# Optimization experiments

Measured on AMD Instinct MI355X. Metric: run time of the kernel, lower is better.

The kernel has to match this reference:

```python
import jax, jax.numpy as jnp
import numpy as np

B, U, C, M = 4096, 1024, 5000, 20

def setup_inputs() -> dict:
    key = jax.random.key(0)
    ks = jax.random.split(key, 9)
    inputs = jax.random.randint(ks[0], (B, 1), 0, C).astype(jnp.int32)
    states = 0.1 * jax.random.normal(ks[1], (B, U + 2), dtype=jnp.float32)
    bias_z = jnp.zeros((U,), jnp.float32)
    recurrent_kernel = 0.02 * jax.random.normal(ks[2], (U, 4 * U), dtype=jnp.float32)
    kernel_c = 0.02 * jax.random.normal(ks[3], (C, 4 * U), dtype=jnp.float32)
    bias = jnp.zeros((3 * U,), jnp.float32)
    kernel_d = 0.1 * jax.random.normal(ks[4], (2, 4 * U), dtype=jnp.float32)
    Wgmm_part1 = 0.05 * jax.random.normal(ks[5], (U, 3 * M), dtype=jnp.float32)
    bgmm_part1 = jnp.zeros((3 * M,), jnp.float32)
    return {"inputs": inputs, "states": states, "bias_z": bias_z,
            "recurrent_kernel": recurrent_kernel, "kernel_c": kernel_c,
            "bias": bias, "kernel_d": kernel_d,
            "Wgmm_part1": Wgmm_part1, "bgmm_part1": bgmm_part1}

def exp_safe(x):
    return jnp.clip(jnp.exp(x), 1e-10, 1e10)

def reference(inputs, states, bias_z, recurrent_kernel, kernel_c, bias,
              kernel_d, Wgmm_part1, bgmm_part1):
    u = bias_z.shape[0]
    h_tm1 = states[:, :-2]          # [B, U]
    _d = states[:, -2:]             # [B, 2]
    ch = inputs[:, 0].astype(jnp.int32)
    # one_hot(ch) @ kernel_c is just a row gather
    pre = kernel_c[ch] + _d @ kernel_d              # [B, 4U]
    # z and r gates share the left operand -> fuse into one matmul
    zr = (h_tm1 @ recurrent_kernel[:, :2 * u] + pre[:, :2 * u]
          + jnp.concatenate([bias_z, bias[:u]]))
    z = jax.nn.sigmoid(zr[:, :u])
    r = jax.nn.sigmoid(zr[:, u:])
    hh = jnp.tanh((r * h_tm1) @ recurrent_kernel[:, 2 * u:3 * u]
                  + pre[:, 2 * u:3 * u] + bias[u:2 * u])
    h = z * h_tm1 + (1.0 - z) * hh
    o = jnp.tanh(h @ recurrent_kernel[:, 3 * u:]
                 + pre[:, 3 * u:] + bias[2 * u:])
    gmm = o @ Wgmm_part1 + bgmm_part1               # [B, 3M]
    _pi, mux, muy = jnp.split(gmm, 3, axis=-1)
    e = exp_safe(_pi)
    pi = e / jnp.sum(e, axis=-1, keepdims=True)
    x_pred = jnp.sum(pi * mux, axis=-1, keepdims=True)
    y_pred = jnp.sum(pi * muy, axis=-1, keepdims=True)
    out = jnp.concatenate([o, pi, mux, muy, x_pred, y_pred], axis=-1)
    new_state = jnp.concatenate([h, x_pred, y_pred], axis=-1)
    return out, new_state
```

## Files before the change

kernel.cpp:

```cpp
#include <hip/hip_runtime.h>

typedef __attribute__((ext_vector_type(8))) short     bf16x8;
typedef __attribute__((ext_vector_type(4))) float     f32x4;
typedef __attribute__((ext_vector_type(2))) float     f32x2;
typedef __attribute__((ext_vector_type(4))) unsigned short u16x4;

#define OUT_STRIDE 1086
#define NS_STRIDE 1026
#define NS_BASE (4096*1086)

__device__ __forceinline__ unsigned short f2bf(float x) {
  unsigned int u = __float_as_uint(x);
  unsigned int r = (u + 0x7FFFu + ((u >> 16) & 1u)) >> 16;
  return (unsigned short)r;
}
__device__ __forceinline__ float bf2f(unsigned short u) {
  union { unsigned int i; float f; } v; v.i = ((unsigned int)u) << 16; return v.f;
}
__device__ __forceinline__ float sigmoidf(float x) { return 1.f / (1.f + expf(-x)); }

__device__ __forceinline__ void gld_lds16(const void* g, void* l) {
  __builtin_amdgcn_global_load_lds((const __attribute__((address_space(1))) void*)g,
                                   (__attribute__((address_space(3))) void*)l, 16, 0, 0);
}

__device__ __forceinline__ void decode_block(int bid, int& m0, int& n0) {
  const int swz = (bid & 7) * 64 + (bid >> 3);
  const int chunk = swz >> 6, l = swz & 63;
  m0 = ((chunk & 3) * 8 + (l >> 3)) * 128;
  n0 = ((chunk >> 2) * 8 + (l & 7)) * 64;
}

__global__ __launch_bounds__(256)
void transposeR(const float* __restrict__ R, unsigned short* __restrict__ Bt) {
  __shared__ float t[64][65];
  const int tx = threadIdx.x & 63, ty = threadIdx.x >> 6;
  const int j0 = blockIdx.x * 64, k0 = blockIdx.y * 64;
#pragma unroll
  for (int i = 0; i < 64; i += 4)
    t[ty + i][tx] = R[(size_t)(k0 + ty + i) * 4096 + j0 + tx];
  __syncthreads();
#pragma unroll
  for (int i = 0; i < 64; i += 4) {
    const int j = ty + i;
    Bt[(size_t)(j0 + j) * 1024 + k0 + tx] = f2bf(t[tx][j]);
  }
}

__global__ __launch_bounds__(256)
void convertH(const float* __restrict__ states, unsigned short* __restrict__ hb) {
  const int idx = blockIdx.x * 256 + threadIdx.x;
  const int b = idx >> 8, u = (idx & 255) * 4;
  const float* sp = states + (size_t)b * 1026 + u;
  f32x2 v0 = *(const f32x2*)sp, v1 = *(const f32x2*)(sp + 2);
  u16x4 w;
  w[0] = f2bf(v0[0]); w[1] = f2bf(v0[1]); w[2] = f2bf(v1[0]); w[3] = f2bf(v1[1]);
  *(u16x4*)&hb[(size_t)b * 1024 + u] = w;
}

__global__ __launch_bounds__(256)
void gemm_zr(const unsigned short* __restrict__ A,
             const unsigned short* __restrict__ Bt,
             const int* __restrict__ chv,
             const float* __restrict__ states,
             const float* __restrict__ kc,
             const float* __restrict__ kd,
             const float* __restrict__ bias_z,
             const float* __restrict__ bias,
             float* __restrict__ zbuf,
             unsigned short* __restrict__ rh) {
  __shared__ unsigned short Al[4][128 * 32];
  __shared__ unsigned short Bzl[4][64 * 32];
  __shared__ unsigned short Brl[4][64 * 32];
  __shared__ int   chs[128];
  __shared__ float d0s[128], d1s[128];

  const int tid = threadIdx.x, lane = tid & 63, wave = tid >> 6;
  int m0, n0;
  decode_block(blockIdx.x, m0, n0);

  if (tid < 128) {
    const int r = m0 + tid;
    chs[tid] = chv[r];
    d0s[tid] = states[(size_t)r * 1026 + 1024];
    d1s[tid] = states[(size_t)r * 1026 + 1025];
  }

  const unsigned short* Ag  = A  + (size_t)m0 * 1024;
  const unsigned short* Bzg = Bt + (size_t)n0 * 1024;
  const unsigned short* Brg = Bt + (size_t)(1024 + n0) * 1024;

  const int c1 = tid + 256;
  const int ar0 = tid >> 2, ak0 = (tid & 3) * 8;
  const int ar1 = c1 >> 2,  ak1 = (c1 & 3) * 8;

  f32x4 accz[2][4] = {}, accr[2][4] = {};
  const int arow = lane & 15, kg = (lane >> 4) * 8;

#define STAGE_ZR(b, kk)                                                        \
  gld_lds16(Ag  + (size_t)ar0 * 1024 + (kk) + ak0, &Al[b][tid * 8]);           \
  gld_lds16(Ag  + (size_t)ar1 * 1024 + (kk) + ak1, &Al[b][c1 * 8]);            \
  gld_lds16(Bzg + (size_t)ar0 * 1024 + (kk) + ak0, &Bzl[b][tid * 8]);          \
  gld_lds16(Brg + (size_t)ar0 * 1024 + (kk) + ak0, &Brl[b][tid * 8]);

  auto compute = [&](int cb) {
    bf16x8 af[2], bzf[4], brf[4];
#pragma unroll
    for (int mi = 0; mi < 2; ++mi)
      af[mi] = *(const bf16x8*)&Al[cb][(wave * 32 + mi * 16 + arow) * 32 + kg];
#pragma unroll
    for (int ni = 0; ni < 4; ++ni) {
      bzf[ni] = *(const bf16x8*)&Bzl[cb][(ni * 16 + arow) * 32 + kg];
      brf[ni] = *(const bf16x8*)&Brl[cb][(ni * 16 + arow) * 32 + kg];
    }
    __builtin_amdgcn_s_setprio(1);
#pragma unroll
    for (int mi = 0; mi < 2; ++mi)
#pragma unroll
      for (int ni = 0; ni < 4; ++ni) {
        accz[mi][ni] = __builtin_amdgcn_mfma_f32_16x16x32_bf16(af[mi], bzf[ni], accz[mi][ni], 0, 0, 0);
        accr[mi][ni] = __builtin_amdgcn_mfma_f32_16x16x32_bf16(af[mi], brf[ni], accr[mi][ni], 0, 0, 0);
      }
    __builtin_amdgcn_s_setprio(0);
  };

  STAGE_ZR(0, 0);
  STAGE_ZR(1, 32);
  for (int t = 0; t < 30; ++t) {
    const int nx = (t + 2) & 3;
    STAGE_ZR(nx, (t + 2) * 32);
    asm volatile("s_waitcnt vmcnt(8)" ::: "memory");
    __builtin_amdgcn_s_barrier();
    asm volatile("" ::: "memory");
    compute(t & 3);
  }
  asm volatile("s_waitcnt vmcnt(4)" ::: "memory");
  __builtin_amdgcn_s_barrier();
  asm volatile("" ::: "memory");
  compute(2);
  asm volatile("s_waitcnt vmcnt(0)" ::: "memory");
  __builtin_amdgcn_s_barrier();
  asm volatile("" ::: "memory");
  compute(3);
#undef STAGE_ZR

#pragma unroll
  for (int mi = 0; mi < 2; ++mi) {
#pragma unroll
    for (int r = 0; r < 4; ++r) {
      const int lrow = wave * 32 + mi * 16 + (lane >> 4) * 4 + r;
      const int grow = m0 + lrow;
      const int ch = chs[lrow];
      const float d0 = d0s[lrow], d1 = d1s[lrow];
      const float* kcrow = kc + (size_t)ch * 4096;
#pragma unroll
      for (int ni = 0; ni < 4; ++ni) {
        const int jc = n0 + ni * 16 + (lane & 15);
        const float vz = accz[mi][ni][r] + kcrow[jc]
                       + d0 * kd[jc] + d1 * kd[4096 + jc] + bias_z[jc];
        const float vr = accr[mi][ni][r] + kcrow[1024 + jc]
                       + d0 * kd[1024 + jc] + d1 * kd[4096 + 1024 + jc] + bias[jc];
        const float z = sigmoidf(vz);
        const float rr = sigmoidf(vr);
        zbuf[(size_t)grow * 1024 + jc] = z;
        rh[(size_t)grow * 1024 + jc] = f2bf(rr * bf2f(A[(size_t)grow * 1024 + jc]));
      }
    }
  }
}

template<int EPI>
__global__ __launch_bounds__(256)
void gemm_k(const unsigned short* __restrict__ A,
            const unsigned short* __restrict__ Bt,
            const int* __restrict__ chv,
            const float* __restrict__ states,
            const float* __restrict__ kc, int colbase,
            const float* __restrict__ kd,
            const float* __restrict__ bias, int biasoff,
            const float* __restrict__ zbuf,
            float* __restrict__ out2,
            unsigned short* __restrict__ hb2) {
  __shared__ unsigned short Al[4][128 * 32];
  __shared__ unsigned short Bl[4][64 * 32];
  __shared__ int   chs[128];
  __shared__ float d0s[128], d1s[128];

  const int tid = threadIdx.x, lane = tid & 63, wave = tid >> 6;
  int m0, n0;
  decode_block(blockIdx.x, m0, n0);

  if (tid < 128) {
    const int r = m0 + tid;
    chs[tid] = chv[r];
    d0s[tid] = states[(size_t)r * 1026 + 1024];
    d1s[tid] = states[(size_t)r * 1026 + 1025];
  }

  const unsigned short* Ag = A  + (size_t)m0 * 1024;
  const unsigned short* Bg = Bt + (size_t)n0 * 1024;

  const int c1 = tid + 256;
  const int ar0 = tid >> 2, ak0 = (tid & 3) * 8;
  const int ar1 = c1 >> 2,  ak1 = (c1 & 3) * 8;

  f32x4 acc[2][4] = {};
  const int arow = lane & 15, kg = (lane >> 4) * 8;

#define STAGE_K(b, kk)                                                         \
  gld_lds16(Ag + (size_t)ar0 * 1024 + (kk) + ak0, &Al[b][tid * 8]);            \
  gld_lds16(Ag + (size_t)ar1 * 1024 + (kk) + ak1, &Al[b][c1 * 8]);             \
  gld_lds16(Bg + (size_t)ar0 * 1024 + (kk) + ak0, &Bl[b][tid * 8]);

  auto compute = [&](int cb) {
    bf16x8 af[2], bfr[4];
#pragma unroll
    for (int mi = 0; mi < 2; ++mi)
      af[mi] = *(const bf16x8*)&Al[cb][(wave * 32 + mi * 16 + arow) * 32 + kg];
#pragma unroll
    for (int ni = 0; ni < 4; ++ni)
      bfr[ni] = *(const bf16x8*)&Bl[cb][(ni * 16 + arow) * 32 + kg];
    __builtin_amdgcn_s_setprio(1);
#pragma unroll
    for (int mi = 0; mi < 2; ++mi)
#pragma unroll
      for (int ni = 0; ni < 4; ++ni)
        acc[mi][ni] = __builtin_amdgcn_mfma_f32_16x16x32_bf16(af[mi], bfr[ni], acc[mi][ni], 0, 0, 0);
    __builtin_amdgcn_s_setprio(0);
  };

  STAGE_K(0, 0);
  STAGE_K(1, 32);
  for (int t = 0; t < 30; ++t) {
    const int nx = (t + 2) & 3;
    STAGE_K(nx, (t + 2) * 32);
    asm volatile("s_waitcnt vmcnt(6)" ::: "memory");
    __builtin_amdgcn_s_barrier();
    asm volatile("" ::: "memory");
    compute(t & 3);
  }
  asm volatile("s_waitcnt vmcnt(3)" ::: "memory");
  __builtin_amdgcn_s_barrier();
  asm volatile("" ::: "memory");
  compute(2);
  asm volatile("s_waitcnt vmcnt(0)" ::: "memory");
  __builtin_amdgcn_s_barrier();
  asm volatile("" ::: "memory");
  compute(3);
#undef STAGE_K

#pragma unroll
  for (int mi = 0; mi < 2; ++mi) {
#pragma unroll
    for (int r = 0; r < 4; ++r) {
      const int lrow = wave * 32 + mi * 16 + (lane >> 4) * 4 + r;
      const int grow = m0 + lrow;
      const int ch = chs[lrow];
      const float d0 = d0s[lrow], d1 = d1s[lrow];
      const float* kcrow = kc + (size_t)ch * 4096 + colbase;
#pragma unroll
      for (int ni = 0; ni < 4; ++ni) {
        const int gcol = n0 + ni * 16 + (lane & 15);
        float v = acc[mi][ni][r] + kcrow[gcol]
                + d0 * kd[colbase + gcol] + d1 * kd[4096 + colbase + gcol]
                + bias[biasoff + gcol];
        if (EPI == 2) {
          const float hh = tanhf(v);
          const float z = zbuf[(size_t)grow * 1024 + gcol];
          const float htm = states[(size_t)grow * 1026 + gcol];
          const float h = z * htm + (1.f - z) * hh;
          out2[(size_t)grow * NS_STRIDE + gcol] = h;
          hb2[(size_t)grow * 1024 + gcol] = f2bf(h);
        } else {
          out2[(size_t)grow * OUT_STRIDE + gcol] = tanhf(v);
        }
      }
    }
  }
}

__global__ __launch_bounds__(512)
void gmm_kernel(const float* __restrict__ obuf,
                const float* __restrict__ Wg,
                const float* __restrict__ bg,
                float* __restrict__ outp,
                float* __restrict__ ns) {
  __shared__ float Wl[128 * 60 + 16];
  __shared__ float ol[8 * 1024];
  const int tid = threadIdx.x;
  const int lane = tid & 63;
  const int wave = tid >> 6;
  const int row0 = blockIdx.x * 8;

  for (int i = tid; i < 4096; i += 512) {
    const int rr = i >> 9, c2 = (i & 511) * 2;
    *(f32x2*)&ol[rr * 1024 + c2] = *(const f32x2*)&obuf[(size_t)(row0 + rr) * OUT_STRIDE + c2];
  }

  float g = 0.f;
  for (int kc0 = 0; kc0 < 1024; kc0 += 128) {
    __syncthreads();
    for (int i = tid; i < 1920; i += 512)
      *(f32x4*)&Wl[i * 4] = *(const f32x4*)&Wg[kc0 * 60 + i * 4];
    __syncthreads();
    const float* orow = &ol[wave * 1024 + kc0];
#pragma unroll 8
    for (int k = 0; k < 128; ++k)
      g = fmaf(orow[k], Wl[k * 60 + lane], g);
  }
  if (lane < 60) g += bg[lane];

  float e = 0.f;
  if (lane < 20) e = fminf(fmaxf(expf(g), 1e-10f), 1e10f);
  float s = e;
#pragma unroll
  for (int m = 1; m < 32; m <<= 1) s += __shfl_xor(s, m, 64);
  const float pi = (lane < 20) ? e / s : 0.f;
  const int src1 = (lane < 20) ? lane + 20 : lane;
  const int src2 = (lane < 20) ? lane + 40 : lane;
  const float mux = __shfl(g, src1, 64);
  const float muy = __shfl(g, src2, 64);
  float px = pi * mux, py = pi * muy;
#pragma unroll
  for (int m = 1; m < 32; m <<= 1) { px += __shfl_xor(px, m, 64); py += __shfl_xor(py, m, 64); }

  const int row = row0 + wave;
  float* orow = outp + (size_t)row * OUT_STRIDE;
  if (lane < 20) orow[1024 + lane] = pi;
  else if (lane < 60) orow[1024 + lane] = g;
  if (lane == 0) {
    orow[1084] = px;
    orow[1085] = py;
    ns[(size_t)row * NS_STRIDE + 1024] = px;
    ns[(size_t)row * NS_STRIDE + 1025] = py;
  }
}

extern "C" void kernel_launch(void* const* d_in, const int* in_sizes, int n_in,
                              void* d_out, int out_size, void* d_ws, size_t ws_size,
                              hipStream_t stream) {
  const int*   chv    = (const int*)d_in[0];
  const float* states = (const float*)d_in[1];
  const float* bias_z = (const float*)d_in[2];
  const float* R      = (const float*)d_in[3];
  const float* kc     = (const float*)d_in[4];
  const float* bias   = (const float*)d_in[5];
  const float* kd     = (const float*)d_in[6];
  const float* Wg     = (const float*)d_in[7];
  const float* bg     = (const float*)d_in[8];
  float* out = (float*)d_out;

  char* ws = (char*)d_ws;
  unsigned short* RbT  = (unsigned short*)ws;
  unsigned short* hb   = (unsigned short*)(ws + 8388608);
  unsigned short* rh   = (unsigned short*)(ws + 16777216);
  unsigned short* hb2  = (unsigned short*)(ws + 25165824);
  float*          zbuf = (float*)(ws + 33554432);

  transposeR<<<dim3(64, 16), 256, 0, stream>>>(R, RbT);
  convertH<<<4096, 256, 0, stream>>>(states, hb);

  gemm_zr<<<512, 256, 0, stream>>>(hb, RbT, chv, states, kc, kd, bias_z, bias, zbuf, rh);

  gemm_k<2><<<512, 256, 0, stream>>>(rh, RbT + (size_t)2048 * 1024,
      chv, states, kc, 2048, kd, bias, 1024, zbuf, out + NS_BASE, hb2);

  gemm_k<3><<<512, 256, 0, stream>>>(hb2, RbT + (size_t)3072 * 1024,
      chv, states, kc, 3072, kd, bias, 2048, nullptr, out, nullptr);

  gmm_kernel<<<512, 512, 0, stream>>>(out, Wg, bg, out, out + NS_BASE);
}
```

Baseline: 328.7 us.

## Compute GMM head with bf16 MFMA using bf16 copy of o and transposed weights

The output-gate GEMM epilogue now also writes a bf16 copy of o into the reused hb buffer. A new prep kernel transposes and pads Wgmm to 64 columns in bf16. The fp32 LDS-based GMM kernel is replaced by an MFMA 16x16x32 kernel that splits K across four waves, reduces the partials through shared memory, and runs the softmax and mixture sums on the MFMA output layout. This targets the scalar FMA cost of the small head GEMM, at the price of bf16 rounding on o and Wgmm and one extra kernel launch.

```diff
diff --git a/kernel.cpp b/kernel.cpp
--- a/kernel.cpp
+++ b/kernel.cpp
@@ -56,6 +56,17 @@
   u16x4 w;
   w[0] = f2bf(v0[0]); w[1] = f2bf(v0[1]); w[2] = f2bf(v1[0]); w[3] = f2bf(v1[1]);
   *(u16x4*)&hb[(size_t)b * 1024 + u] = w;
+}
+
+__global__ __launch_bounds__(256)
+void prep_wgt(const float* __restrict__ Wg, unsigned short* __restrict__ WgT) {
+  const int idx = blockIdx.x * 256 + threadIdx.x;
+  const int c = idx & 63, kq = idx >> 6;
+#pragma unroll
+  for (int j = 0; j < 4; ++j) {
+    const int k = kq * 4 + j;
+    WgT[(size_t)c * 1024 + k] = (c < 60) ? f2bf(Wg[(size_t)k * 60 + c]) : (unsigned short)0;
+  }
 }
 
 __global__ __launch_bounds__(256)
@@ -272,67 +283,104 @@
           out2[(size_t)grow * NS_STRIDE + gcol] = h;
           hb2[(size_t)grow * 1024 + gcol] = f2bf(h);
         } else {
-          out2[(size_t)grow * OUT_STRIDE + gcol] = tanhf(v);
+          const float o = tanhf(v);
+          out2[(size_t)grow * OUT_STRIDE + gcol] = o;
+          hb2[(size_t)grow * 1024 + gcol] = f2bf(o);
         }
       }
     }
   }
 }
 
-__global__ __launch_bounds__(512)
-void gmm_kernel(const float* __restrict__ obuf,
-                const float* __restrict__ Wg,
-                const float* __restrict__ bg,
-                float* __restrict__ outp,
-                float* __restrict__ ns) {
-  __shared__ float Wl[128 * 60 + 16];
-  __shared__ float ol[8 * 1024];
-  const int tid = threadIdx.x;
-  const int lane = tid & 63;
-  const int wave = tid >> 6;
-  const int row0 = blockIdx.x * 8;
-
-  for (int i = tid; i < 4096; i += 512) {
-    const int rr = i >> 9, c2 = (i & 511) * 2;
-    *(f32x2*)&ol[rr * 1024 + c2] = *(const f32x2*)&obuf[(size_t)(row0 + rr) * OUT_STRIDE + c2];
-  }
-
-  float g = 0.f;
-  for (int kc0 = 0; kc0 < 1024; kc0 += 128) {
-    __syncthreads();
-    for (int i = tid; i < 1920; i += 512)
-      *(f32x4*)&Wl[i * 4] = *(const f32x4*)&Wg[kc0 * 60 + i * 4];
-    __syncthreads();
-    const float* orow = &ol[wave * 1024 + kc0];
-#pragma unroll 8
-    for (int k = 0; k < 128; ++k)
-      g = fmaf(orow[k], Wl[k * 60 + lane], g);
-  }
-  if (lane < 60) g += bg[lane];
-
-  float e = 0.f;
-  if (lane < 20) e = fminf(fmaxf(expf(g), 1e-10f), 1e10f);
-  float s = e;
-#pragma unroll
-  for (int m = 1; m < 32; m <<= 1) s += __shfl_xor(s, m, 64);
-  const float pi = (lane < 20) ? e / s : 0.f;
-  const int src1 = (lane < 20) ? lane + 20 : lane;
-  const int src2 = (lane < 20) ? lane + 40 : lane;
-  const float mux = __shfl(g, src1, 64);
-  const float muy = __shfl(g, src2, 64);
-  float px = pi * mux, py = pi * muy;
-#pragma unroll
-  for (int m = 1; m < 32; m <<= 1) { px += __shfl_xor(px, m, 64); py += __shfl_xor(py, m, 64); }
-
-  const int row = row0 + wave;
-  float* orow = outp + (size_t)row * OUT_STRIDE;
-  if (lane < 20) orow[1024 + lane] = pi;
-  else if (lane < 60) orow[1024 + lane] = g;
-  if (lane == 0) {
-    orow[1084] = px;
-    orow[1085] = py;
-    ns[(size_t)row * NS_STRIDE + 1024] = px;
-    ns[(size_t)row * NS_STRIDE + 1025] = py;
+__global__ __launch_bounds__(256)
+void gmm2(const unsigned short* __restrict__ ob,
+          const unsigned short* __restrict__ WgT,
+          const float* __restrict__ bg,
+          float* __restrict__ outp,
+          float* __restrict__ ns) {
+  __shared__ float red[3 * 16 * 64];
+  const int tid = threadIdx.x, lane = tid & 63, wave = tid >> 6;
+  const int arow = lane & 15, q = lane >> 4;
+  const int r0 = blockIdx.x * 16;
+
+  const unsigned short* Al = ob  + (size_t)(r0 + arow) * 1024 + q * 8 + wave * 256;
+  const unsigned short* Bl = WgT + (size_t)arow * 1024 + q * 8 + wave * 256;
+
+  f32x4 acc[4] = {};
+#pragma unroll
+  for (int t = 0; t < 8; ++t) {
+    const bf16x8 af = *(const bf16x8*)(Al + t * 32);
+#pragma unroll
+    for (int ni = 0; ni < 4; ++ni) {
+      const bf16x8 bf_ = *(const bf16x8*)(Bl + (size_t)ni * 16 * 1024 + t * 32);
+      acc[ni] = __builtin_amdgcn_mfma_f32_16x16x32_bf16(af, bf_, acc[ni], 0, 0, 0);
+    }
+  }
+
+  if (wave) {
+#pragma unroll
+    for (int ni = 0; ni < 4; ++ni)
+#pragma unroll
+      for (int i = 0; i < 4; ++i)
+        red[(wave - 1) * 1024 + (ni * 4 + i) * 64 + lane] = acc[ni][i];
+  }
+  __syncthreads();
+  if (wave == 0) {
+#pragma unroll
+    for (int w = 0; w < 3; ++w)
+#pragma unroll
+      for (int ni = 0; ni < 4; ++ni)
+#pragma unroll
+        for (int i = 0; i < 4; ++i)
+          acc[ni][i] += red[w * 1024 + (ni * 4 + i) * 64 + lane];
+
+    const int gb = lane & 48;
+#pragma unroll
+    for (int i = 0; i < 4; ++i) {
+      float g0 = acc[0][i] + bg[arow];
+      float g1 = acc[1][i] + ((16 + arow < 60) ? bg[16 + arow] : 0.f);
+      float g2 = acc[2][i] + ((32 + arow < 60) ? bg[32 + arow] : 0.f);
+      float g3 = acc[3][i] + ((48 + arow < 60) ? bg[48 + arow] : 0.f);
+
+      const float e0 = fminf(fmaxf(expf(g0), 1e-10f), 1e10f);
+      const float e1 = (arow < 4) ? fminf(fmaxf(expf(g1), 1e-10f), 1e10f) : 0.f;
+      float s = e0 + e1;
+#pragma unroll
+      for (int m = 1; m < 16; m <<= 1) s += __shfl_xor(s, m, 64);
+      const float pi0 = e0 / s;
+      const float pi1 = e1 / s;
+
+      const float t1 = __shfl(g1, gb | ((arow + 4) & 15), 64);
+      const float t2 = __shfl(g2, gb | ((arow + 4) & 15), 64);
+      const float muxA = (arow < 12) ? t1 : t2;
+      const float muxB = t2;
+      const float u1 = __shfl(g2, gb | ((arow + 8) & 15), 64);
+      const float u2 = __shfl(g3, gb | ((arow + 8) & 15), 64);
+      const float muyA = (arow < 8) ? u1 : u2;
+      const float muyB = u2;
+
+      float px = pi0 * muxA + ((arow < 4) ? pi1 * muxB : 0.f);
+      float py = pi0 * muyA + ((arow < 4) ? pi1 * muyB : 0.f);
+#pragma unroll
+      for (int m = 1; m < 16; m <<= 1) {
+        px += __shfl_xor(px, m, 64);
+        py += __shfl_xor(py, m, 64);
+      }
+
+      const int row = r0 + q * 4 + i;
+      float* orow = outp + (size_t)row * OUT_STRIDE;
+      orow[1024 + arow] = pi0;
+      if (arow < 4)  orow[1040 + arow] = pi1;
+      if (arow >= 4) orow[1040 + arow] = g1;
+      orow[1056 + arow] = g2;
+      if (arow < 12) orow[1072 + arow] = g3;
+      if (arow == 0) {
+        orow[1084] = px;
+        orow[1085] = py;
+        ns[(size_t)row * NS_STRIDE + 1024] = px;
+        ns[(size_t)row * NS_STRIDE + 1025] = py;
+      }
+    }
   }
 }
 
@@ -356,9 +404,11 @@
   unsigned short* rh   = (unsigned short*)(ws + 16777216);
   unsigned short* hb2  = (unsigned short*)(ws + 25165824);
   float*          zbuf = (float*)(ws + 33554432);
+  unsigned short* WgT  = (unsigned short*)(ws + 50331648);
 
   transposeR<<<dim3(64, 16), 256, 0, stream>>>(R, RbT);
   convertH<<<4096, 256, 0, stream>>>(states, hb);
+  prep_wgt<<<64, 256, 0, stream>>>(Wg, WgT);
 
   gemm_zr<<<512, 256, 0, stream>>>(hb, RbT, chv, states, kc, kd, bias_z, bias, zbuf, rh);
 
@@ -366,7 +416,7 @@
       chv, states, kc, 2048, kd, bias, 1024, zbuf, out + NS_BASE, hb2);
 
   gemm_k<3><<<512, 256, 0, stream>>>(hb2, RbT + (size_t)3072 * 1024,
-      chv, states, kc, 3072, kd, bias, 2048, nullptr, out, nullptr);
-
-  gmm_kernel<<<512, 512, 0, stream>>>(out, Wg, bg, out, out + NS_BASE);
-}
+      chv, states, kc, 3072, kd, bias, 2048, nullptr, out, hb);
+
+  gmm2<<<256, 256, 0, stream>>>(hb, WgT, bg, out, out + NS_BASE);
+}
```

After: 310.2 us. 5.6% less time.
